# Kernel tuning notes

Measured on AMD Instinct MI355X. Metric: run time of the kernel, lower is better.

Reference implementation:

```python
import jax, jax.numpy as jnp
import numpy as np

B, T, C, H = 4, 4096, 768, 64  # batch, seq, embed_size, head_size


def setup_inputs() -> dict:
    key = jax.random.key(0)
    kx, kq, kk, kv = jax.random.split(key, 4)
    s = 1.0 / np.sqrt(C)
    return {
        "x": jax.random.normal(kx, (B, T, C), dtype=jnp.float32),
        "Wq": jax.random.normal(kq, (C, H), dtype=jnp.float32) * s,
        "Wk": jax.random.normal(kk, (C, H), dtype=jnp.float32) * s,
        "Wv": jax.random.normal(kv, (C, H), dtype=jnp.float32) * s,
    }


def reference(x, Wq, Wk, Wv):
    Bx, Tx, Cx = x.shape
    Q = x @ Wq  # [B, T, H]
    K = x @ Wk
    V = x @ Wv
    # NOTE: original scales by sqrt(C) = sqrt(embed_size), not head_size
    scores = jnp.einsum('bqh,bkh->bqk', Q, K) / jnp.sqrt(jnp.asarray(Cx, x.dtype))
    causal = jnp.tril(jnp.ones((Tx, Tx), dtype=bool))
    scores = jnp.where(causal, scores, -jnp.inf)
    weights = jax.nn.softmax(scores, axis=-1)
    # dropout = identity in eval mode
    return jnp.einsum('bqk,bkh->bqh', weights, V)
```

## Files before the change

kernel.cpp:

```cpp
#include <hip/hip_runtime.h>

typedef __bf16 bf16x8 __attribute__((ext_vector_type(8)));
typedef float f32x4 __attribute__((ext_vector_type(4)));

#define MFMA16(a,b,c) __builtin_amdgcn_mfma_f32_16x16x32_bf16(a,b,c,0,0,0)

__device__ __forceinline__ unsigned short f2b(float x){
  __bf16 b = (__bf16)x;
  return __builtin_bit_cast(unsigned short, b);
}

__device__ __forceinline__ void gld16(const void* g, void* l){
  __builtin_amdgcn_global_load_lds(
      (const __attribute__((address_space(1))) unsigned int*)g,
      (__attribute__((address_space(3))) unsigned int*)l, 16, 0, 0);
}

__global__ __launch_bounds__(256) void pack_w(const float* __restrict__ Wq,
                                              const float* __restrict__ Wk,
                                              const float* __restrict__ Wv,
                                              unsigned short* __restrict__ Wt){
  int idx = blockIdx.x*256 + threadIdx.x;
  int n = idx/768, c = idx - n*768;
  const float* W = (n < 64) ? Wq : ((n < 128) ? Wk : Wv);
  Wt[n*768 + c] = f2b(W[c*64 + (n & 63)]);
}

__global__ __launch_bounds__(256,2) void qkv_proj(const float* __restrict__ x,
                                                  const unsigned short* __restrict__ Wt,
                                                  unsigned short* __restrict__ Qb,
                                                  unsigned short* __restrict__ Kb,
                                                  unsigned short* __restrict__ Vt){
  __shared__ __attribute__((aligned(16))) float Xl[2][32*64];
  __shared__ __attribute__((aligned(16))) unsigned short Wl[2][192*64];
  const int tid = threadIdx.x;
  const int w = tid>>6, l = tid&63, quad = l>>4, lr = l&15;
  const int row0 = blockIdx.x*32;

  auto stage = [&](int kk, int buf){
#pragma unroll
    for(int i=0;i<2;i++){
      int n = (w*2+i)*4 + (l>>4);
      int sc = (l&15) ^ (n&15);
      gld16(x + (size_t)(row0+n)*768 + kk*64 + sc*4, &Xl[buf][(w*2+i)*256]);
    }
#pragma unroll
    for(int i=0;i<6;i++){
      int gr0 = (w*6+i)*8;
      int n = gr0 + (l>>3);
      int sc = (l&7) ^ (l>>3);
      gld16(Wt + (size_t)n*768 + kk*64 + sc*8, &Wl[buf][gr0*64]);
    }
  };

  f32x4 acc[2][3];
#pragma unroll
  for(int mt=0;mt<2;mt++)
#pragma unroll
    for(int nt=0;nt<3;nt++) acc[mt][nt] = (f32x4)0.0f;

  stage(0, 0);
  int buf = 0;
  for(int kk=0; kk<12; kk++){
    __syncthreads();
    if(kk+1 < 12) stage(kk+1, buf^1);
    bf16x8 a[2][2];
#pragma unroll
    for(int mt=0;mt<2;mt++){
#pragma unroll
      for(int ks=0;ks<2;ks++){
        int c = ks*8 + quad*2;
        f32x4 v0 = *(const f32x4*)&Xl[buf][(mt*16+lr)*64 + ((c   ^ lr)&15)*4];
        f32x4 v1 = *(const f32x4*)&Xl[buf][(mt*16+lr)*64 + (((c+1)^ lr)&15)*4];
#pragma unroll
        for(int jj=0;jj<4;jj++){ a[mt][ks][jj] = (__bf16)v0[jj]; a[mt][ks][4+jj] = (__bf16)v1[jj]; }
      }
    }
#pragma unroll
    for(int nt=0;nt<3;nt++){
#pragma unroll
      for(int ks=0;ks<2;ks++){
        int n = w*48 + nt*16 + lr;
        int q = ks*4 + quad;
        bf16x8 bfr = *(const bf16x8*)&Wl[buf][n*64 + ((q ^ (lr&7))&7)*8];
#pragma unroll
        for(int mt=0;mt<2;mt++) acc[mt][nt] = MFMA16(a[mt][ks], bfr, acc[mt][nt]);
      }
    }
    buf ^= 1;
  }
  const int b_ = row0>>12;
  const float sc = 0.03608439182435161f;
#pragma unroll
  for(int mt=0;mt<2;mt++){
    const int t0 = (row0 & 4095) + mt*16 + quad*4;
#pragma unroll
    for(int nt=0;nt<3;nt++){
      int g = w*48 + nt*16 + lr;
      if(g < 64){
#pragma unroll
        for(int r=0;r<4;r++) Qb[((size_t)(b_*4096 + t0 + r))*64 + g] = f2b(acc[mt][nt][r]*sc);
      } else if(g < 128){
#pragma unroll
        for(int r=0;r<4;r++) Kb[((size_t)(b_*4096 + t0 + r))*64 + (g-64)] = f2b(acc[mt][nt][r]);
      } else {
        ushort4 pk;
        pk.x = f2b(acc[mt][nt][0]); pk.y = f2b(acc[mt][nt][1]);
        pk.z = f2b(acc[mt][nt][2]); pk.w = f2b(acc[mt][nt][3]);
        *(ushort4*)&Vt[((size_t)(b_*64 + (g-128)))*4096 + t0] = pk;
      }
    }
  }
}

__device__ __forceinline__ void attn_stage(const unsigned short* kbp, const unsigned short* vbp,
                                           int kt, int w, int r8, int cj,
                                           unsigned short* Kl, unsigned short* Vl){
#pragma unroll
  for(int i=0;i<2;i++){
    int row = w*16 + i*8 + r8;
    int gc = cj ^ r8;
    gld16(kbp + ((size_t)(kt*64 + row))*64 + gc*8, Kl + (w*16 + i*8)*64);
    gld16(vbp + ((size_t)row)*4096 + kt*64 + gc*8, Vl + (w*16 + i*8)*64);
  }
}

__global__ __launch_bounds__(256,2) void attn(const unsigned short* __restrict__ Qb,
                                              const unsigned short* __restrict__ Kb,
                                              const unsigned short* __restrict__ Vt,
                                              float* __restrict__ Opart,
                                              float* __restrict__ Rpart){
  __shared__ __attribute__((aligned(16))) unsigned short Kl[2][64*64];
  __shared__ __attribute__((aligned(16))) unsigned short Vl[2][64*64];
  __shared__ __attribute__((aligned(16))) unsigned short Pl[4][16*72];
  const int tid = threadIdx.x;
  const int w = tid>>6, l = tid&63, quad = l>>4, lr = l&15;
  const int j = blockIdx.x;
  const int qt = 63 - (j>>3);
  const int sub = j & 7, b = sub>>1, sh = sub&1;
  const int q0 = qt*64;
  const int nfull = qt;
  const int r8 = l>>3, cj = l&7;
  const unsigned short* qp = Qb + ((size_t)(b*4096 + q0 + w*16 + lr))*64 + quad*8;
  const bf16x8 aq0 = *(const bf16x8*)qp;
  const bf16x8 aq1 = *(const bf16x8*)(qp + 32);
  const int qg = q0 + w*16 + quad*4;
  f32x4 o_[4];
#pragma unroll
  for(int i=0;i<4;i++) o_[i] = (f32x4)0.0f;
  float rs[4] = {0.f,0.f,0.f,0.f};
  const unsigned short* kbp = Kb + ((size_t)b*4096)*64;
  const unsigned short* vbp = Vt + ((size_t)b*64)*4096;
  unsigned short* pw = &Pl[w][0];
  const int lx = lr & 7;

  int cur = 0;
  if(sh <= nfull) attn_stage(kbp, vbp, sh, w, r8, cj, Kl[0], Vl[0]);
  for(int kt = sh; kt <= nfull; kt += 2){
    __syncthreads();
    if(kt+2 <= nfull) attn_stage(kbp, vbp, kt+2, w, r8, cj, Kl[cur^1], Vl[cur^1]);
    f32x4 s4[4];
#pragma unroll
    for(int ct=0;ct<4;ct++){
      int base = (ct*16+lr)*64;
      bf16x8 b0 = *(const bf16x8*)&Kl[cur][base + ((quad   ^ lx)<<3)];
      bf16x8 b1 = *(const bf16x8*)&Kl[cur][base + (((4+quad)^ lx)<<3)];
      f32x4 z = (f32x4)0.0f;
      z = MFMA16(aq0, b0, z);
      s4[ct] = MFMA16(aq1, b1, z);
    }
    if(kt == nfull){
#pragma unroll
      for(int ct=0;ct<4;ct++){
        int kg = kt*64 + ct*16 + lr;
#pragma unroll
        for(int r=0;r<4;r++){
          float p = (kg <= qg + r) ? __expf(s4[ct][r]) : 0.0f;
          rs[r] += p;
          pw[(quad*4+r)*72 + ct*16 + lr] = f2b(p);
        }
      }
    } else {
#pragma unroll
      for(int ct=0;ct<4;ct++){
#pragma unroll
        for(int r=0;r<4;r++){
          float p = __expf(s4[ct][r]);
          rs[r] += p;
          pw[(quad*4+r)*72 + ct*16 + lr] = f2b(p);
        }
      }
    }
#pragma unroll
    for(int ks=0;ks<2;ks++){
      bf16x8 ap = *(const bf16x8*)&pw[lr*72 + ks*32 + quad*8];
#pragma unroll
      for(int nt=0;nt<4;nt++){
        bf16x8 bv = *(const bf16x8*)&Vl[cur][(nt*16+lr)*64 + (((ks*4+quad)^lx)<<3)];
        o_[nt] = MFMA16(ap, bv, o_[nt]);
      }
    }
    cur ^= 1;
  }
  const size_t slab = (size_t)(sh*4 + b)*4096;
#pragma unroll
  for(int r=0;r<4;r++){
    float t = rs[r];
#pragma unroll
    for(int off=1; off<16; off<<=1) t += __shfl_xor(t, off, 16);
    int rowt = q0 + w*16 + quad*4 + r;
    if(lr == 0) Rpart[slab + rowt] = t;
#pragma unroll
    for(int nt=0;nt<4;nt++)
      Opart[(slab + rowt)*64 + nt*16 + lr] = o_[nt][r];
  }
}

__global__ __launch_bounds__(256) void combine(const float* __restrict__ Opart,
                                               const float* __restrict__ Rpart,
                                               float* __restrict__ out){
  int i = blockIdx.x*256 + threadIdx.x;
  size_t off = (size_t)i*4;
  int rowt = (int)(off >> 6);
  float rsum = Rpart[rowt] + Rpart[16384 + rowt];
  f32x4 a = *(const f32x4*)(Opart + off);
  f32x4 c = *(const f32x4*)(Opart + (size_t)16384*64 + off);
  float inv = 1.0f / rsum;
  f32x4 v;
#pragma unroll
  for(int k2=0;k2<4;k2++) v[k2] = (a[k2]+c[k2])*inv;
  *(f32x4*)(out + off) = v;
}

extern "C" void kernel_launch(void* const* d_in, const int* in_sizes, int n_in,
                              void* d_out, int out_size, void* d_ws, size_t ws_size,
                              hipStream_t stream){
  const float* x  = (const float*)d_in[0];
  const float* Wq = (const float*)d_in[1];
  const float* Wk = (const float*)d_in[2];
  const float* Wv = (const float*)d_in[3];
  float* out = (float*)d_out;
  char* ws = (char*)d_ws;
  unsigned short* Wt = (unsigned short*)(ws);
  unsigned short* Qb = (unsigned short*)(ws + 0x080000);
  unsigned short* Kb = (unsigned short*)(ws + 0x280000);
  unsigned short* Vt = (unsigned short*)(ws + 0x480000);
  float* Opart = (float*)(ws + 0x680000);
  float* Rpart = (float*)(ws + 0xE80000);
  hipLaunchKernelGGL(pack_w,   dim3(576),  dim3(256), 0, stream, Wq, Wk, Wv, Wt);
  hipLaunchKernelGGL(qkv_proj, dim3(512),  dim3(256), 0, stream, x, Wt, Qb, Kb, Vt);
  hipLaunchKernelGGL(attn,     dim3(512),  dim3(256), 0, stream, Qb, Kb, Vt, Opart, Rpart);
  hipLaunchKernelGGL(combine,  dim3(1024), dim3(256), 0, stream, Opart, Rpart, out);
}
```

Measured before the change: 138.3 us.

## Use 128-row query tiles with KV-chunk split and bf16 partial outputs

The attention kernel now processes 128 query rows per block, two 16-row MFMA tiles per wave, so each K/V tile loaded into LDS is reused for twice as many queries. The key range is split into chunks of up to 8 tiles per block over a 144x4 grid, ordered longest-first, instead of a fixed even/odd two-way split. Partial outputs are stored in bf16, and the combine kernel sums a variable number of partials per row. This cuts K/V reload traffic and balances causal work better, at the cost of more register pressure, more partial writes and lower precision in the partials.

```diff
diff --git a/kernel.cpp b/kernel.cpp
--- a/kernel.cpp
+++ b/kernel.cpp
@@ -8,6 +8,9 @@
 __device__ __forceinline__ unsigned short f2b(float x){
   __bf16 b = (__bf16)x;
   return __builtin_bit_cast(unsigned short, b);
+}
+__device__ __forceinline__ float b2f(unsigned short u){
+  return __builtin_bit_cast(float, ((unsigned)u)<<16);
 }
 
 __device__ __forceinline__ void gld16(const void* g, void* l){
@@ -128,108 +131,138 @@
 __global__ __launch_bounds__(256,2) void attn(const unsigned short* __restrict__ Qb,
                                               const unsigned short* __restrict__ Kb,
                                               const unsigned short* __restrict__ Vt,
-                                              float* __restrict__ Opart,
+                                              unsigned short* __restrict__ Opart,
                                               float* __restrict__ Rpart){
   __shared__ __attribute__((aligned(16))) unsigned short Kl[2][64*64];
   __shared__ __attribute__((aligned(16))) unsigned short Vl[2][64*64];
-  __shared__ __attribute__((aligned(16))) unsigned short Pl[4][16*72];
+  __shared__ __attribute__((aligned(16))) unsigned short Pl[4][32*72];
   const int tid = threadIdx.x;
   const int w = tid>>6, l = tid&63, quad = l>>4, lr = l&15;
-  const int j = blockIdx.x;
-  const int qt = 63 - (j>>3);
-  const int sub = j & 7, b = sub>>1, sh = sub&1;
-  const int q0 = qt*64;
-  const int nfull = qt;
+  const int xx = 143 - blockIdx.x;
+  int i = 0, accu = 0;
+  while(true){ int c = (i+4)>>2; if(accu + c > xx) break; accu += c; i++; }
+  const int r = xx - accu;
+  const int b = blockIdx.y;
+  const int q0 = i*128;
+  const int lo = r*8;
+  const int hi = min(lo+8, 2*i+2);
+  const int diag0 = 2*i;
   const int r8 = l>>3, cj = l&7;
-  const unsigned short* qp = Qb + ((size_t)(b*4096 + q0 + w*16 + lr))*64 + quad*8;
-  const bf16x8 aq0 = *(const bf16x8*)qp;
-  const bf16x8 aq1 = *(const bf16x8*)(qp + 32);
-  const int qg = q0 + w*16 + quad*4;
-  f32x4 o_[4];
-#pragma unroll
-  for(int i=0;i<4;i++) o_[i] = (f32x4)0.0f;
-  float rs[4] = {0.f,0.f,0.f,0.f};
+  const int lx = lr & 7;
+  bf16x8 aq[2][2];
+#pragma unroll
+  for(int m=0;m<2;m++){
+    const unsigned short* qp = Qb + ((size_t)(b*4096 + q0 + w*32 + m*16 + lr))*64 + quad*8;
+    aq[m][0] = *(const bf16x8*)qp;
+    aq[m][1] = *(const bf16x8*)(qp + 32);
+  }
+  f32x4 o_[2][4];
+#pragma unroll
+  for(int m=0;m<2;m++)
+#pragma unroll
+    for(int nt=0;nt<4;nt++) o_[m][nt] = (f32x4)0.0f;
+  float rs[2][4] = {{0.f,0.f,0.f,0.f},{0.f,0.f,0.f,0.f}};
   const unsigned short* kbp = Kb + ((size_t)b*4096)*64;
   const unsigned short* vbp = Vt + ((size_t)b*64)*4096;
   unsigned short* pw = &Pl[w][0];
-  const int lx = lr & 7;
-
+
+  attn_stage(kbp, vbp, lo, w, r8, cj, Kl[0], Vl[0]);
   int cur = 0;
-  if(sh <= nfull) attn_stage(kbp, vbp, sh, w, r8, cj, Kl[0], Vl[0]);
-  for(int kt = sh; kt <= nfull; kt += 2){
+  for(int kt = lo; kt < hi; kt++){
     __syncthreads();
-    if(kt+2 <= nfull) attn_stage(kbp, vbp, kt+2, w, r8, cj, Kl[cur^1], Vl[cur^1]);
-    f32x4 s4[4];
+    if(kt+1 < hi) attn_stage(kbp, vbp, kt+1, w, r8, cj, Kl[cur^1], Vl[cur^1]);
+    f32x4 s4[2][4];
 #pragma unroll
     for(int ct=0;ct<4;ct++){
       int base = (ct*16+lr)*64;
-      bf16x8 b0 = *(const bf16x8*)&Kl[cur][base + ((quad   ^ lx)<<3)];
+      bf16x8 b0 = *(const bf16x8*)&Kl[cur][base + ((quad    ^ lx)<<3)];
       bf16x8 b1 = *(const bf16x8*)&Kl[cur][base + (((4+quad)^ lx)<<3)];
-      f32x4 z = (f32x4)0.0f;
-      z = MFMA16(aq0, b0, z);
-      s4[ct] = MFMA16(aq1, b1, z);
-    }
-    if(kt == nfull){
-#pragma unroll
-      for(int ct=0;ct<4;ct++){
-        int kg = kt*64 + ct*16 + lr;
-#pragma unroll
-        for(int r=0;r<4;r++){
-          float p = (kg <= qg + r) ? __expf(s4[ct][r]) : 0.0f;
-          rs[r] += p;
-          pw[(quad*4+r)*72 + ct*16 + lr] = f2b(p);
+#pragma unroll
+      for(int m=0;m<2;m++){
+        f32x4 z = (f32x4)0.0f;
+        z = MFMA16(aq[m][0], b0, z);
+        s4[m][ct] = MFMA16(aq[m][1], b1, z);
+      }
+    }
+    if(kt >= diag0){
+#pragma unroll
+      for(int m=0;m<2;m++){
+        int qg = q0 + w*32 + m*16 + quad*4;
+#pragma unroll
+        for(int ct=0;ct<4;ct++){
+          int kg = kt*64 + ct*16 + lr;
+#pragma unroll
+          for(int rr=0;rr<4;rr++){
+            float p = (kg <= qg + rr) ? __expf(s4[m][ct][rr]) : 0.0f;
+            rs[m][rr] += p;
+            pw[(m*16+quad*4+rr)*72 + ct*16 + lr] = f2b(p);
+          }
         }
       }
     } else {
 #pragma unroll
-      for(int ct=0;ct<4;ct++){
-#pragma unroll
-        for(int r=0;r<4;r++){
-          float p = __expf(s4[ct][r]);
-          rs[r] += p;
-          pw[(quad*4+r)*72 + ct*16 + lr] = f2b(p);
+      for(int m=0;m<2;m++){
+#pragma unroll
+        for(int ct=0;ct<4;ct++){
+#pragma unroll
+          for(int rr=0;rr<4;rr++){
+            float p = __expf(s4[m][ct][rr]);
+            rs[m][rr] += p;
+            pw[(m*16+quad*4+rr)*72 + ct*16 + lr] = f2b(p);
+          }
         }
       }
     }
 #pragma unroll
     for(int ks=0;ks<2;ks++){
-      bf16x8 ap = *(const bf16x8*)&pw[lr*72 + ks*32 + quad*8];
+      bf16x8 ap[2];
+#pragma unroll
+      for(int m=0;m<2;m++) ap[m] = *(const bf16x8*)&pw[(m*16+lr)*72 + ks*32 + quad*8];
 #pragma unroll
       for(int nt=0;nt<4;nt++){
         bf16x8 bv = *(const bf16x8*)&Vl[cur][(nt*16+lr)*64 + (((ks*4+quad)^lx)<<3)];
-        o_[nt] = MFMA16(ap, bv, o_[nt]);
+#pragma unroll
+        for(int m=0;m<2;m++) o_[m][nt] = MFMA16(ap[m], bv, o_[m][nt]);
       }
     }
     cur ^= 1;
   }
-  const size_t slab = (size_t)(sh*4 + b)*4096;
-#pragma unroll
-  for(int r=0;r<4;r++){
-    float t = rs[r];
-#pragma unroll
-    for(int off=1; off<16; off<<=1) t += __shfl_xor(t, off, 16);
-    int rowt = q0 + w*16 + quad*4 + r;
-    if(lr == 0) Rpart[slab + rowt] = t;
-#pragma unroll
-    for(int nt=0;nt<4;nt++)
-      Opart[(slab + rowt)*64 + nt*16 + lr] = o_[nt][r];
-  }
-}
-
-__global__ __launch_bounds__(256) void combine(const float* __restrict__ Opart,
+  const int slab = r*4 + b;
+#pragma unroll
+  for(int m=0;m<2;m++){
+#pragma unroll
+    for(int rr=0;rr<4;rr++){
+      float t = rs[m][rr];
+#pragma unroll
+      for(int off=1; off<16; off<<=1) t += __shfl_xor(t, off, 16);
+      int row = q0 + w*32 + m*16 + quad*4 + rr;
+      if(lr == 0) Rpart[slab*4096 + row] = t;
+#pragma unroll
+      for(int nt=0;nt<4;nt++)
+        Opart[((size_t)(slab*4096 + row))*64 + nt*16 + lr] = f2b(o_[m][nt][rr]);
+    }
+  }
+}
+
+__global__ __launch_bounds__(256) void combine(const unsigned short* __restrict__ Opart,
                                                const float* __restrict__ Rpart,
                                                float* __restrict__ out){
-  int i = blockIdx.x*256 + threadIdx.x;
-  size_t off = (size_t)i*4;
-  int rowt = (int)(off >> 6);
-  float rsum = Rpart[rowt] + Rpart[16384 + rowt];
-  f32x4 a = *(const f32x4*)(Opart + off);
-  f32x4 c = *(const f32x4*)(Opart + (size_t)16384*64 + off);
-  float inv = 1.0f / rsum;
-  f32x4 v;
-#pragma unroll
-  for(int k2=0;k2<4;k2++) v[k2] = (a[k2]+c[k2])*inv;
-  *(f32x4*)(out + off) = v;
+  int gid = blockIdx.x*256 + threadIdx.x;
+  int cg = gid & 15;
+  int t  = (gid >> 4) & 4095;
+  int b  = gid >> 16;
+  int i  = t >> 7;
+  int np = (i + 4) >> 2;
+  float o0=0.f, o1=0.f, o2=0.f, o3=0.f, rsum=0.f;
+  for(int r=0; r<np; r++){
+    int slab = r*4 + b;
+    rsum += Rpart[slab*4096 + t];
+    ushort4 u = *(const ushort4*)(Opart + ((size_t)(slab*4096 + t))*64 + cg*4);
+    o0 += b2f(u.x); o1 += b2f(u.y); o2 += b2f(u.z); o3 += b2f(u.w);
+  }
+  float inv = 1.0f/rsum;
+  f32x4 v; v[0]=o0*inv; v[1]=o1*inv; v[2]=o2*inv; v[3]=o3*inv;
+  *(f32x4*)(out + ((size_t)(b*4096 + t))*64 + cg*4) = v;
 }
 
 extern "C" void kernel_launch(void* const* d_in, const int* in_sizes, int n_in,
@@ -245,10 +278,10 @@
   unsigned short* Qb = (unsigned short*)(ws + 0x080000);
   unsigned short* Kb = (unsigned short*)(ws + 0x280000);
   unsigned short* Vt = (unsigned short*)(ws + 0x480000);
-  float* Opart = (float*)(ws + 0x680000);
-  float* Rpart = (float*)(ws + 0xE80000);
-  hipLaunchKernelGGL(pack_w,   dim3(576),  dim3(256), 0, stream, Wq, Wk, Wv, Wt);
-  hipLaunchKernelGGL(qkv_proj, dim3(512),  dim3(256), 0, stream, x, Wt, Qb, Kb, Vt);
-  hipLaunchKernelGGL(attn,     dim3(512),  dim3(256), 0, stream, Qb, Kb, Vt, Opart, Rpart);
-  hipLaunchKernelGGL(combine,  dim3(1024), dim3(256), 0, stream, Opart, Rpart, out);
-}
+  unsigned short* Opart = (unsigned short*)(ws + 0x680000);
+  float* Rpart = (float*)(ws + 0x1680000);
+  hipLaunchKernelGGL(pack_w,   dim3(576),     dim3(256), 0, stream, Wq, Wk, Wv, Wt);
+  hipLaunchKernelGGL(qkv_proj, dim3(512),     dim3(256), 0, stream, x, Wt, Qb, Kb, Vt);
+  hipLaunchKernelGGL(attn,     dim3(144, 4),  dim3(256), 0, stream, Qb, Kb, Vt, Opart, Rpart);
+  hipLaunchKernelGGL(combine,  dim3(1024),    dim3(256), 0, stream, Opart, Rpart, out);
+}
```

Result: faster. 128.3 us (-7.2%).
